# Performance work log

Measured on AMD Instinct MI355X. Metric: run time of the kernel, lower is better.

Reference implementation:

```python
import jax, jax.numpy as jnp
import numpy as np

V, ENC, D, E = 10000, 2048, 512, 512
B, L = 128, 64


def setup_inputs() -> dict:
    key = jax.random.key(0)
    ks = jax.random.split(key, 12)
    s = lambda *sh: 1.0 / np.sqrt(sh[-1])
    return {
        "global_feats": jax.random.normal(ks[0], (B, ENC), jnp.float32),
        "encoded_captions": jax.random.randint(ks[1], (B, L), 0, V, jnp.int64),
        "caption_lengths": jax.random.randint(ks[2], (B,), 1, L, jnp.int64),
        "W_embed": jax.random.normal(ks[3], (V, E), jnp.float32) * 0.02,
        "W_init": jax.random.normal(ks[4], (D, ENC), jnp.float32) * s(ENC),
        "b_init": jnp.zeros((D,), jnp.float32),
        "W_ih": jax.random.normal(ks[5], (3 * D, E), jnp.float32) * s(E),
        "W_hh": jax.random.normal(ks[6], (3 * D, D), jnp.float32) * s(D),
        "b_ih": jnp.zeros((3 * D,), jnp.float32),
        "b_hh": jnp.zeros((3 * D,), jnp.float32),
        "W_fc": jax.random.normal(ks[7], (V, D), jnp.float32) * s(D),
        "b_fc": jnp.zeros((V,), jnp.float32),
    }


def reference(global_feats, encoded_captions, caption_lengths,
              W_embed, W_init, b_init, W_ih, W_hh, b_ih, b_hh, W_fc, b_fc):
    # init_hidden: h0 = tanh(Linear(global_feats))  -> (B, D)
    h0 = jnp.tanh(global_feats @ W_init.T + b_init)

    # teacher forcing over timesteps 0..L-2 (PyTorch GRU gate order: r, z, n)
    emb = W_embed[encoded_captions[:, : L - 1]]          # (B, L-1, E)
    gi = jnp.einsum('ble,ge->blg', emb, W_ih) + b_ih     # (B, L-1, 3D) precomputed input gates
    gi = jnp.swapaxes(gi, 0, 1)                          # (L-1, B, 3D) scan over time

    def step(h, gi_t):
        gh = h @ W_hh.T + b_hh                           # (B, 3D)
        i_r, i_z, i_n = jnp.split(gi_t, 3, axis=-1)
        h_r, h_z, h_n = jnp.split(gh, 3, axis=-1)
        r = jax.nn.sigmoid(i_r + h_r)
        z = jax.nn.sigmoid(i_z + h_z)
        n = jnp.tanh(i_n + r * h_n)
        h_new = (1.0 - z) * n + z * h
        return h_new, h_new

    _, hs = jax.lax.scan(step, h0, gi)                   # hs: (L-1, B, D)
    # dropout is identity in eval/reference mode
    logits = jnp.einsum('lbd,vd->blv', hs, W_fc) + b_fc  # (B, L-1, V)
    return logits, caption_lengths - 1
```

## Files before the change

kernel.cpp:

```cpp
#include <hip/hip_runtime.h>
#include <hip/hip_bf16.h>

#define V_    10000
#define ENC_  2048
#define D_    512
#define B_    128
#define L_    64
#define T_    63
#define M_    (B_ * L_ - B_)
#define G_    (3 * D_)
#define LOGITS_SZ ((long)M_ * V_)
#define SCAN_NB 64

typedef __bf16 bf16x8_t __attribute__((ext_vector_type(8)));
typedef float  f32x4_t  __attribute__((ext_vector_type(4)));
typedef short  s16x8_t  __attribute__((ext_vector_type(8)));
typedef unsigned long long ull_t;

typedef __attribute__((address_space(3))) char*       lds_cptr_t;
typedef const __attribute__((address_space(1))) char* glb_cptr_t;

__device__ __forceinline__ void gload_lds16(const void* g, void* l) {
  __builtin_amdgcn_global_load_lds((glb_cptr_t)g, (lds_cptr_t)l, 16, 0, 0);
}
__device__ __forceinline__ float bf2f(short s) {
  return __uint_as_float(((unsigned)(unsigned short)s) << 16);
}
__device__ __forceinline__ short f2bf(float f) {
  __hip_bfloat16 h = __float2bfloat16(f);
  return *reinterpret_cast<short*>(&h);
}
__device__ __forceinline__ s16x8_t cvt8(const float* p) {
  f32x4_t lo = *reinterpret_cast<const f32x4_t*>(p);
  f32x4_t hi = *reinterpret_cast<const f32x4_t*>(p + 4);
  s16x8_t r;
#pragma unroll
  for (int e = 0; e < 4; e++) { r[e] = f2bf(lo[e]); r[4 + e] = f2bf(hi[e]); }
  return r;
}
__device__ __forceinline__ float sigmoidf_(float x) {
  return 1.0f / (1.0f + __expf(-x));
}
__device__ __forceinline__ bf16x8_t lds_frag(const short* p) {
  return __builtin_bit_cast(bf16x8_t, *reinterpret_cast<const s16x8_t*>(p));
}

__global__ void GG_cvt6(const float* __restrict__ whh, __hip_bfloat16* __restrict__ dwhh,
                        const float* __restrict__ wih, __hip_bfloat16* __restrict__ dwih,
                        const float* __restrict__ wemb, __hip_bfloat16* __restrict__ dwemb,
                        const float* __restrict__ winit, __hip_bfloat16* __restrict__ dwinit,
                        const float* __restrict__ gf, __hip_bfloat16* __restrict__ dgf,
                        const float* __restrict__ wfc, __hip_bfloat16* __restrict__ dwfc) {
  const int i = blockIdx.x * blockDim.x + threadIdx.x;
  const float* s; __hip_bfloat16* d; int off;
  if (i < 98304)        { s = whh;   d = dwhh;   off = i; }
  else if (i < 196608)  { s = wih;   d = dwih;   off = i - 98304; }
  else if (i < 836608)  { s = wemb;  d = dwemb;  off = i - 196608; }
  else if (i < 967680)  { s = winit; d = dwinit; off = i - 836608; }
  else if (i < 1000448) { s = gf;    d = dgf;    off = i - 967680; }
  else {
    if (dwfc == nullptr || i >= 1640448) return;
    s = wfc; d = dwfc; off = i - 1000448;
  }
  s16x8_t v = cvt8(s + (long)off * 8);
  *reinterpret_cast<s16x8_t*>(d + (long)off * 8) = v;
}

__global__ __launch_bounds__(256) void GG_prep(
    const __hip_bfloat16* __restrict__ gfB,
    const __hip_bfloat16* __restrict__ WinitB,
    const float* __restrict__ binit,
    __hip_bfloat16* __restrict__ hfull,
    const __hip_bfloat16* __restrict__ WembB,
    const int* __restrict__ cap,
    const __hip_bfloat16* __restrict__ WihB,
    const float* __restrict__ bih,
    __hip_bfloat16* __restrict__ giC,
    const int* __restrict__ lens,
    float* __restrict__ out) {
  __shared__ short smem[2 * 128 * 64];
  short* sA = smem;
  short* sB = smem + 128 * 64;
  const int lane = threadIdx.x & 63;
  const int wave = threadIdx.x >> 6;
  const int srow = lane >> 3;
  const int scolz = ((lane & 7) ^ (srow & 7)) * 8;
  const int fr = lane & 15;
  const int g4 = lane >> 4;
  const int wm = (wave >> 1) * 64;
  const int wn = (wave & 1) * 64;

  if (blockIdx.x >= 760) {
    if (threadIdx.x < B_) out[LOGITS_SZ + threadIdx.x] = (float)(lens[threadIdx.x] - 1);
    return;
  }

  f32x4_t acc[4][4] = {};

  if (blockIdx.x < 4) {
    const int n0 = blockIdx.x * 128;
    const __hip_bfloat16* aptr[4];
    const __hip_bfloat16* bptr[4];
#pragma unroll
    for (int i = 0; i < 4; i++) {
      const int r = (wave * 4 + i) * 8 + srow;
      aptr[i] = gfB + (long)r * ENC_ + scolz;
      bptr[i] = WinitB + (long)(n0 + r) * ENC_ + scolz;
    }
    for (int kt = 0; kt < 32; kt++) {
      __syncthreads();
#pragma unroll
      for (int i = 0; i < 4; i++) {
        const int chunk = wave * 4 + i;
        gload_lds16(aptr[i] + kt * 64, sA + chunk * 512);
        gload_lds16(bptr[i] + kt * 64, sB + chunk * 512);
      }
      __syncthreads();
#pragma unroll
      for (int kk = 0; kk < 2; kk++) {
        const int gsw = ((kk * 4 + g4) ^ (fr & 7)) * 8;
        bf16x8_t a[4], b[4];
#pragma unroll
        for (int i = 0; i < 4; i++) {
          a[i] = lds_frag(sA + (wm + i * 16 + fr) * 64 + gsw);
          b[i] = lds_frag(sB + (wn + i * 16 + fr) * 64 + gsw);
        }
#pragma unroll
        for (int i = 0; i < 4; i++)
#pragma unroll
          for (int j = 0; j < 4; j++)
            acc[i][j] = __builtin_amdgcn_mfma_f32_16x16x32_bf16(a[i], b[j], acc[i][j], 0, 0, 0);
      }
    }
    const int fq = lane >> 4;
#pragma unroll
    for (int j = 0; j < 4; j++) {
      const int n = n0 + wn + j * 16 + fr;
      const float bv = binit[n];
#pragma unroll
      for (int i = 0; i < 4; i++)
#pragma unroll
        for (int rr = 0; rr < 4; rr++) {
          const int m = wm + i * 16 + fq * 4 + rr;
          hfull[(long)m * 64 * 512 + n] = __float2bfloat16(tanhf(acc[i][j][rr] + bv));
        }
    }
    return;
  }

  const int flat = blockIdx.x - 4;
  const int m0 = (flat / 12) * 128;
  const int n0 = (flat % 12) * 128;
  const __hip_bfloat16* aptr[4];
  const __hip_bfloat16* bptr[4];
#pragma unroll
  for (int i = 0; i < 4; i++) {
    const int r = (wave * 4 + i) * 8 + srow;
    const int bt = m0 + r;
    const int bb = bt / 63;
    const int tt = bt - bb * 63;
    aptr[i] = WembB + (long)cap[bb * L_ + tt] * 512 + scolz;
    bptr[i] = WihB + (long)(n0 + r) * 512 + scolz;
  }
  for (int kt = 0; kt < 8; kt++) {
    __syncthreads();
#pragma unroll
    for (int i = 0; i < 4; i++) {
      const int chunk = wave * 4 + i;
      gload_lds16(aptr[i] + kt * 64, sA + chunk * 512);
      gload_lds16(bptr[i] + kt * 64, sB + chunk * 512);
    }
    __syncthreads();
#pragma unroll
    for (int kk = 0; kk < 2; kk++) {
      const int gsw = ((kk * 4 + g4) ^ (fr & 7)) * 8;
      bf16x8_t a[4], b[4];
#pragma unroll
      for (int i = 0; i < 4; i++) {
        a[i] = lds_frag(sA + (wm + i * 16 + fr) * 64 + gsw);
        b[i] = lds_frag(sB + (wn + i * 16 + fr) * 64 + gsw);
      }
#pragma unroll
      for (int i = 0; i < 4; i++)
#pragma unroll
        for (int j = 0; j < 4; j++)
          acc[i][j] = __builtin_amdgcn_mfma_f32_16x16x32_bf16(a[i], b[j], acc[i][j], 0, 0, 0);
    }
  }
  const int fq = lane >> 4;
#pragma unroll
  for (int j = 0; j < 4; j++) {
    const int n = n0 + wn + j * 16 + fr;
    const float bv = bih[n];
#pragma unroll
    for (int i = 0; i < 4; i++)
#pragma unroll
      for (int rr = 0; rr < 4; rr++) {
        const int m = m0 + wm + i * 16 + fq * 4 + rr;
        giC[(long)m * G_ + n] = __float2bfloat16(acc[i][j][rr] + bv);
      }
  }
}

template <bool BBF16>
__global__ __launch_bounds__(512) void GG_gemm_logits(
    const __hip_bfloat16* __restrict__ hfull,
    const void* __restrict__ Bsrc,
    const float* __restrict__ bias,
    float* __restrict__ C) {
  const int flat = blockIdx.x;
  const int xcd = flat & 7;
  const int s = flat >> 3;
  const int col = xcd * 5 + s % 5;
  const int row = s / 5;
  const int m0 = row * 128;
  const int n0 = col * 256;

  __shared__ short sA[128 * 64];
  __shared__ short sB[256 * 64];
  const int lane = threadIdx.x & 63;
  const int wave = threadIdx.x >> 6;
  const int srow = lane >> 3;
  const int scol  = (lane & 7) * 8;
  const int scolz = ((lane & 7) ^ (srow & 7)) * 8;

  f32x4_t acc[4][4] = {};

  const __hip_bfloat16* aptr[2];
#pragma unroll
  for (int i = 0; i < 2; i++) {
    const int r = (wave + i * 8) * 8 + srow;
    const int m = m0 + r;
    const int bb = m / 63;
    const int tt = m - bb * 63;
    aptr[i] = hfull + ((long)bb * 64 + tt + 1) * 512 + scolz;
  }
  const __hip_bfloat16* bptrB[4];
  const float* bptrF[4];
#pragma unroll
  for (int i = 0; i < 4; i++) {
    int nrow = n0 + (wave + i * 8) * 8 + srow;
    nrow = (nrow < V_) ? nrow : (V_ - 1);
    if constexpr (BBF16) bptrB[i] = (const __hip_bfloat16*)Bsrc + (long)nrow * 512 + scolz;
    else                 bptrF[i] = (const float*)Bsrc + (long)nrow * 512 + scol;
  }

  const int wm = (wave >> 2) * 64;
  const int wn = (wave & 3) * 64;
  const int fr = lane & 15;
  const int g4 = lane >> 4;

  for (int kt = 0; kt < 8; kt++) {
    s16x8_t vb[4];
    if constexpr (!BBF16) {
#pragma unroll
      for (int i = 0; i < 4; i++) vb[i] = cvt8(bptrF[i] + kt * 64);
    }
    __syncthreads();
#pragma unroll
    for (int i = 0; i < 2; i++)
      gload_lds16(aptr[i] + kt * 64, sA + (wave + i * 8) * 512);
#pragma unroll
    for (int i = 0; i < 4; i++) {
      if constexpr (BBF16)
        gload_lds16(bptrB[i] + kt * 64, sB + (wave + i * 8) * 512);
      else
        *reinterpret_cast<s16x8_t*>(
            sB + (wave + i * 8) * 512 + srow * 64 + (((lane & 7) ^ (srow & 7)) * 8)) = vb[i];
    }
    __syncthreads();
#pragma unroll
    for (int kk = 0; kk < 2; kk++) {
      const int gsw = ((kk * 4 + g4) ^ (fr & 7)) * 8;
      bf16x8_t a[4], b[4];
#pragma unroll
      for (int i = 0; i < 4; i++) {
        a[i] = lds_frag(sA + (wm + i * 16 + fr) * 64 + gsw);
        b[i] = lds_frag(sB + (wn + i * 16 + fr) * 64 + gsw);
      }
#pragma unroll
      for (int i = 0; i < 4; i++)
#pragma unroll
        for (int j = 0; j < 4; j++)
          acc[i][j] = __builtin_amdgcn_mfma_f32_16x16x32_bf16(a[i], b[j], acc[i][j], 0, 0, 0);
    }
  }

  const int fq = lane >> 4;
#pragma unroll
  for (int j = 0; j < 4; j++) {
    const int n = n0 + wn + j * 16 + fr;
    if (n >= V_) continue;
    const float bv = bias[n];
#pragma unroll
    for (int i = 0; i < 4; i++)
#pragma unroll
      for (int rr = 0; rr < 4; rr++) {
        const int m = m0 + wm + i * 16 + fq * 4 + rr;
        C[(long)m * V_ + n] = acc[i][j][rr] + bv;
      }
  }
}

__global__ __launch_bounds__(256) void GG_scan_persist(
    __hip_bfloat16* __restrict__ hfull,
    const __hip_bfloat16* __restrict__ gi,
    const __hip_bfloat16* __restrict__ WhhB,
    const float* __restrict__ bhh,
    int* __restrict__ flagbase) {
  __shared__ short sW[48 * 512];
  const int lane = threadIdx.x & 63;
  const int wave = threadIdx.x >> 6;
  const int strip = blockIdx.x & 31;
  const int half  = blockIdx.x >> 5;
  const int d0 = strip * 16;
  const int fr = lane & 15;
  const int g4 = lane >> 4;
  int* myflags = flagbase + half * 32;

  for (int rr = wave; rr < 48; rr += 4) {
    const int grow = (rr >> 4) * 512 + d0 + (rr & 15);
    gload_lds16(WhhB + (long)grow * 512 + (lane ^ (rr & 7)) * 8, sW + rr * 512);
  }

  const int dd = d0 + fr;
  const int bbase = half * 64 + wave * 16 + g4 * 4;
  const float br_ = bhh[dd], bz_ = bhh[512 + dd], bn_ = bhh[1024 + dd];
  const short* gis = (const short*)gi;

  const int arow = half * 64 + wave * 16 + fr;
  const ull_t abase0 =
      (ull_t)hfull + ((ull_t)arow * 64 * 512 + (unsigned)(g4 * 8)) * 2ull;

  ull_t sbase[4];
  const short* gp0[4];
#pragma unroll
  for (int rr = 0; rr < 4; rr++) {
    sbase[rr] = (ull_t)hfull +
                ((ull_t)(bbase + rr) * 64 * 512 + (unsigned)dd) * 2ull;
    gp0[rr] = gis + (long)(bbase + rr) * T_ * G_ + dd;
  }

  unsigned cr[4], cz[4], cn[4];
  float hp[4];
#pragma unroll
  for (int rr = 0; rr < 4; rr++) {
    cr[rr] = (unsigned short)gp0[rr][0];
    cz[rr] = (unsigned short)gp0[rr][512];
    cn[rr] = (unsigned short)gp0[rr][1024];
    hp[rr] = bf2f(*(const short*)&hfull[((long)(bbase + rr) * 64) * 512 + dd]);
  }

  asm volatile("s_waitcnt vmcnt(0)" ::: "memory");
  __syncthreads();

  for (int t = 0; t < T_; t++) {
    if (t > 0) {
      while (true) {
        const int v = __hip_atomic_load(&myflags[lane & 31], __ATOMIC_RELAXED,
                                        __HIP_MEMORY_SCOPE_SYSTEM);
        if (__all(v >= t)) break;
        __builtin_amdgcn_s_sleep(1);
      }
    }

    const ull_t ab = abase0 + (ull_t)t * 1024ull;
    f32x4_t a[16];
#define ALOAD(IDX, OFF)                                                        \
    asm volatile("global_load_dwordx4 %0, %1, off offset:" #OFF " sc0 sc1"     \
                 : "=v"(a[IDX]) : "v"(ab));
    ALOAD(0, 0)    ALOAD(1, 64)   ALOAD(2, 128)  ALOAD(3, 192)
    ALOAD(4, 256)  ALOAD(5, 320)  ALOAD(6, 384)  ALOAD(7, 448)
    ALOAD(8, 512)  ALOAD(9, 576)  ALOAD(10, 640) ALOAD(11, 704)
    ALOAD(12, 768) ALOAD(13, 832) ALOAD(14, 896) ALOAD(15, 960)
#undef ALOAD

    const int tp = (t < T_ - 1) ? (t + 1) : (T_ - 1);
    unsigned nr[4], nz[4], nn[4];
#pragma unroll
    for (int rr = 0; rr < 4; rr++) {
      const short* gp = gp0[rr] + (long)tp * G_;
      asm volatile("global_load_ushort %0, %1, off"             : "=v"(nr[rr]) : "v"(gp));
      asm volatile("global_load_ushort %0, %1, off offset:1024" : "=v"(nz[rr]) : "v"(gp));
      asm volatile("global_load_ushort %0, %1, off offset:2048" : "=v"(nn[rr]) : "v"(gp));
    }

    asm volatile("s_waitcnt vmcnt(12)" ::: "memory");
    __builtin_amdgcn_sched_barrier(0);

    f32x4_t acc[3] = {};
#pragma unroll
    for (int kt = 0; kt < 16; kt++) {
      const bf16x8_t afr = __builtin_bit_cast(bf16x8_t, a[kt]);
      const int gsw = ((kt * 4 + g4) ^ (fr & 7)) * 8;
      bf16x8_t bfr[3];
#pragma unroll
      for (int j = 0; j < 3; j++) bfr[j] = lds_frag(sW + (j * 16 + fr) * 512 + gsw);
#pragma unroll
      for (int j = 0; j < 3; j++)
        acc[j] = __builtin_amdgcn_mfma_f32_16x16x32_bf16(afr, bfr[j], acc[j], 0, 0, 0);
    }

#pragma unroll
    for (int rr = 0; rr < 4; rr++) {
      const float rg = sigmoidf_(bf2f((short)cr[rr]) + acc[0][rr] + br_);
      const float zg = sigmoidf_(bf2f((short)cz[rr]) + acc[1][rr] + bz_);
      const float ng = tanhf(bf2f((short)cn[rr]) + rg * (acc[2][rr] + bn_));
      const short hnb = f2bf((1.f - zg) * ng + zg * hp[rr]);
      hp[rr] = bf2f(hnb);
      const ull_t saddr = sbase[rr] + (ull_t)(t + 1) * 1024ull;
      const unsigned int val = (unsigned short)hnb;
      asm volatile("global_store_short %0, %1, off sc0 sc1"
                   :: "v"(saddr), "v"(val) : "memory");
    }

    asm volatile("s_waitcnt vmcnt(0)" ::: "memory");
    __builtin_amdgcn_sched_barrier(0);
#pragma unroll
    for (int rr = 0; rr < 4; rr++) { cr[rr] = nr[rr]; cz[rr] = nz[rr]; cn[rr] = nn[rr]; }

    if (t < T_ - 1) {
      __syncthreads();
      if (threadIdx.x == 0)
        __hip_atomic_store(&myflags[strip], t + 1, __ATOMIC_RELAXED,
                           __HIP_MEMORY_SCOPE_SYSTEM);
    }
  }
}

extern "C" void kernel_launch(void* const* d_in, const int* in_sizes, int n_in,
                              void* d_out, int out_size, void* d_ws, size_t ws_size,
                              hipStream_t stream) {
  const float* gf      = (const float*)d_in[0];
  const int*   cap     = (const int*)d_in[1];
  const int*   lens    = (const int*)d_in[2];
  const float* W_embed = (const float*)d_in[3];
  const float* W_init  = (const float*)d_in[4];
  const float* b_init  = (const float*)d_in[5];
  const float* W_ih    = (const float*)d_in[6];
  const float* W_hh    = (const float*)d_in[7];
  const float* b_ih    = (const float*)d_in[8];
  const float* b_hh    = (const float*)d_in[9];
  const float* W_fc    = (const float*)d_in[10];
  const float* b_fc    = (const float*)d_in[11];
  float* out = (float*)d_out;

  char* ob = (char*)d_out;
  __hip_bfloat16* gi_ws  = (__hip_bfloat16*)ob;
  __hip_bfloat16* WhhB   = (__hip_bfloat16*)(ob + 25165824);
  __hip_bfloat16* WihB   = (__hip_bfloat16*)(ob + 27262976);
  __hip_bfloat16* WembB  = (__hip_bfloat16*)(ob + 29360128);
  __hip_bfloat16* WinitB = (__hip_bfloat16*)(ob + 40894464);
  __hip_bfloat16* gfB    = (__hip_bfloat16*)(ob + 43253760);

  __hip_bfloat16* hfull = (__hip_bfloat16*)d_ws;
  __hip_bfloat16* WfcB  = (__hip_bfloat16*)((char*)d_ws + 8388608);
  const bool big_ws = ws_size >= (size_t)(8388608 + 10240000 + 256);
  int* flags = (int*)((char*)d_ws + (big_ws ? 18628608 : 8388608));

  hipMemsetAsync(flags, 0, 256, stream);

  GG_cvt6<<<dim3(6408), 256, 0, stream>>>(W_hh, WhhB, W_ih, WihB, W_embed, WembB,
                                          W_init, WinitB, gf, gfB,
                                          W_fc, big_ws ? WfcB : nullptr);

  GG_prep<<<dim3(761), 256, 0, stream>>>(gfB, WinitB, b_init, hfull,
                                         WembB, cap, WihB, b_ih, gi_ws, lens, out);

  GG_scan_persist<<<dim3(SCAN_NB), 256, 0, stream>>>(hfull, gi_ws, WhhB, b_hh, flags);

  if (big_ws)
    GG_gemm_logits<true><<<dim3(2520), 512, 0, stream>>>(hfull, WfcB, b_fc, out);
  else
    GG_gemm_logits<false><<<dim3(2520), 512, 0, stream>>>(hfull, W_fc, b_fc, out);
}
```

Measured before the change: 492.6 us.

## Fuse input-gate GEMM, h0 init and GRU scan into one persistent kernel

Merges the prep kernel (h0 init GEMM and gi projection GEMM) and the persistent scan into a single launch. gi is re-laid out time-major (t, b, gate), and each timestep's gi tiles publish a per-timestep counter, so scan blocks can start once h0 and gi for step 0 are ready and overlap the remaining gi GEMM with the recurrence. This removes one launch boundary and the wait for the whole gi GEMM to finish. In exchange it adds spin-waits and LLC-coherent loads and stores, and it relies on the 64 scan blocks (the lowest block indices) being co-resident with the producer blocks to avoid deadlock.

Measured after the change: 541.4 us. 1.1x slower.

```diff
diff --git a/kernel.cpp b/kernel.cpp
--- a/kernel.cpp
+++ b/kernel.cpp
@@ -10,7 +10,10 @@
 #define M_    (B_ * L_ - B_)
 #define G_    (3 * D_)
 #define LOGITS_SZ ((long)M_ * V_)
-#define SCAN_NB 64
+#define NB_SCAN 64
+#define NB_GI   756
+#define NB_H0   4
+#define NB_ALL  (NB_SCAN + NB_GI + NB_H0 + 1)
 
 typedef __bf16 bf16x8_t __attribute__((ext_vector_type(8)));
 typedef float  f32x4_t  __attribute__((ext_vector_type(4)));
@@ -43,6 +46,15 @@
 }
 __device__ __forceinline__ bf16x8_t lds_frag(const short* p) {
   return __builtin_bit_cast(bf16x8_t, *reinterpret_cast<const s16x8_t*>(p));
+}
+__device__ __forceinline__ void store_short_llc(ull_t addr, unsigned val) {
+  asm volatile("global_store_short %0, %1, off sc0 sc1"
+               :: "v"(addr), "v"(val) : "memory");
+}
+__device__ __forceinline__ unsigned load_ushort_llc(const void* p) {
+  unsigned v;
+  asm volatile("global_load_ushort %0, %1, off sc0 sc1" : "=v"(v) : "v"(p));
+  return v;
 }
 
 __global__ void GG_cvt6(const float* __restrict__ whh, __hip_bfloat16* __restrict__ dwhh,
@@ -66,142 +78,6 @@
   *reinterpret_cast<s16x8_t*>(d + (long)off * 8) = v;
 }
 
-__global__ __launch_bounds__(256) void GG_prep(
-    const __hip_bfloat16* __restrict__ gfB,
-    const __hip_bfloat16* __restrict__ WinitB,
-    const float* __restrict__ binit,
-    __hip_bfloat16* __restrict__ hfull,
-    const __hip_bfloat16* __restrict__ WembB,
-    const int* __restrict__ cap,
-    const __hip_bfloat16* __restrict__ WihB,
-    const float* __restrict__ bih,
-    __hip_bfloat16* __restrict__ giC,
-    const int* __restrict__ lens,
-    float* __restrict__ out) {
-  __shared__ short smem[2 * 128 * 64];
-  short* sA = smem;
-  short* sB = smem + 128 * 64;
-  const int lane = threadIdx.x & 63;
-  const int wave = threadIdx.x >> 6;
-  const int srow = lane >> 3;
-  const int scolz = ((lane & 7) ^ (srow & 7)) * 8;
-  const int fr = lane & 15;
-  const int g4 = lane >> 4;
-  const int wm = (wave >> 1) * 64;
-  const int wn = (wave & 1) * 64;
-
-  if (blockIdx.x >= 760) {
-    if (threadIdx.x < B_) out[LOGITS_SZ + threadIdx.x] = (float)(lens[threadIdx.x] - 1);
-    return;
-  }
-
-  f32x4_t acc[4][4] = {};
-
-  if (blockIdx.x < 4) {
-    const int n0 = blockIdx.x * 128;
-    const __hip_bfloat16* aptr[4];
-    const __hip_bfloat16* bptr[4];
-#pragma unroll
-    for (int i = 0; i < 4; i++) {
-      const int r = (wave * 4 + i) * 8 + srow;
-      aptr[i] = gfB + (long)r * ENC_ + scolz;
-      bptr[i] = WinitB + (long)(n0 + r) * ENC_ + scolz;
-    }
-    for (int kt = 0; kt < 32; kt++) {
-      __syncthreads();
-#pragma unroll
-      for (int i = 0; i < 4; i++) {
-        const int chunk = wave * 4 + i;
-        gload_lds16(aptr[i] + kt * 64, sA + chunk * 512);
-        gload_lds16(bptr[i] + kt * 64, sB + chunk * 512);
-      }
-      __syncthreads();
-#pragma unroll
-      for (int kk = 0; kk < 2; kk++) {
-        const int gsw = ((kk * 4 + g4) ^ (fr & 7)) * 8;
-        bf16x8_t a[4], b[4];
-#pragma unroll
-        for (int i = 0; i < 4; i++) {
-          a[i] = lds_frag(sA + (wm + i * 16 + fr) * 64 + gsw);
-          b[i] = lds_frag(sB + (wn + i * 16 + fr) * 64 + gsw);
-        }
-#pragma unroll
-        for (int i = 0; i < 4; i++)
-#pragma unroll
-          for (int j = 0; j < 4; j++)
-            acc[i][j] = __builtin_amdgcn_mfma_f32_16x16x32_bf16(a[i], b[j], acc[i][j], 0, 0, 0);
-      }
-    }
-    const int fq = lane >> 4;
-#pragma unroll
-    for (int j = 0; j < 4; j++) {
-      const int n = n0 + wn + j * 16 + fr;
-      const float bv = binit[n];
-#pragma unroll
-      for (int i = 0; i < 4; i++)
-#pragma unroll
-        for (int rr = 0; rr < 4; rr++) {
-          const int m = wm + i * 16 + fq * 4 + rr;
-          hfull[(long)m * 64 * 512 + n] = __float2bfloat16(tanhf(acc[i][j][rr] + bv));
-        }
-    }
-    return;
-  }
-
-  const int flat = blockIdx.x - 4;
-  const int m0 = (flat / 12) * 128;
-  const int n0 = (flat % 12) * 128;
-  const __hip_bfloat16* aptr[4];
-  const __hip_bfloat16* bptr[4];
-#pragma unroll
-  for (int i = 0; i < 4; i++) {
-    const int r = (wave * 4 + i) * 8 + srow;
-    const int bt = m0 + r;
-    const int bb = bt / 63;
-    const int tt = bt - bb * 63;
-    aptr[i] = WembB + (long)cap[bb * L_ + tt] * 512 + scolz;
-    bptr[i] = WihB + (long)(n0 + r) * 512 + scolz;
-  }
-  for (int kt = 0; kt < 8; kt++) {
-    __syncthreads();
-#pragma unroll
-    for (int i = 0; i < 4; i++) {
-      const int chunk = wave * 4 + i;
-      gload_lds16(aptr[i] + kt * 64, sA + chunk * 512);
-      gload_lds16(bptr[i] + kt * 64, sB + chunk * 512);
-    }
-    __syncthreads();
-#pragma unroll
-    for (int kk = 0; kk < 2; kk++) {
-      const int gsw = ((kk * 4 + g4) ^ (fr & 7)) * 8;
-      bf16x8_t a[4], b[4];
-#pragma unroll
-      for (int i = 0; i < 4; i++) {
-        a[i] = lds_frag(sA + (wm + i * 16 + fr) * 64 + gsw);
-        b[i] = lds_frag(sB + (wn + i * 16 + fr) * 64 + gsw);
-      }
-#pragma unroll
-      for (int i = 0; i < 4; i++)
-#pragma unroll
-        for (int j = 0; j < 4; j++)
-          acc[i][j] = __builtin_amdgcn_mfma_f32_16x16x32_bf16(a[i], b[j], acc[i][j], 0, 0, 0);
-    }
-  }
-  const int fq = lane >> 4;
-#pragma unroll
-  for (int j = 0; j < 4; j++) {
-    const int n = n0 + wn + j * 16 + fr;
-    const float bv = bih[n];
-#pragma unroll
-    for (int i = 0; i < 4; i++)
-#pragma unroll
-      for (int rr = 0; rr < 4; rr++) {
-        const int m = m0 + wm + i * 16 + fq * 4 + rr;
-        giC[(long)m * G_ + n] = __float2bfloat16(acc[i][j][rr] + bv);
-      }
-  }
-}
-
 template <bool BBF16>
 __global__ __launch_bounds__(512) void GG_gemm_logits(
     const __hip_bfloat16* __restrict__ hfull,
@@ -302,130 +178,287 @@
   }
 }
 
-__global__ __launch_bounds__(256) void GG_scan_persist(
+__global__ __launch_bounds__(256) void GG_mega(
     __hip_bfloat16* __restrict__ hfull,
-    const __hip_bfloat16* __restrict__ gi,
+    __hip_bfloat16* __restrict__ gi,
     const __hip_bfloat16* __restrict__ WhhB,
     const float* __restrict__ bhh,
-    int* __restrict__ flagbase) {
-  __shared__ short sW[48 * 512];
+    int* __restrict__ flags,
+    const __hip_bfloat16* __restrict__ gfB,
+    const __hip_bfloat16* __restrict__ WinitB,
+    const float* __restrict__ binit,
+    const __hip_bfloat16* __restrict__ WembB,
+    const int* __restrict__ cap,
+    const __hip_bfloat16* __restrict__ WihB,
+    const float* __restrict__ bih,
+    const int* __restrict__ lens,
+    float* __restrict__ out) {
+  __shared__ short smem[48 * 512];
   const int lane = threadIdx.x & 63;
   const int wave = threadIdx.x >> 6;
-  const int strip = blockIdx.x & 31;
-  const int half  = blockIdx.x >> 5;
-  const int d0 = strip * 16;
   const int fr = lane & 15;
   const int g4 = lane >> 4;
-  int* myflags = flagbase + half * 32;
-
-  for (int rr = wave; rr < 48; rr += 4) {
-    const int grow = (rr >> 4) * 512 + d0 + (rr & 15);
-    gload_lds16(WhhB + (long)grow * 512 + (lane ^ (rr & 7)) * 8, sW + rr * 512);
-  }
-
-  const int dd = d0 + fr;
-  const int bbase = half * 64 + wave * 16 + g4 * 4;
-  const float br_ = bhh[dd], bz_ = bhh[512 + dd], bn_ = bhh[1024 + dd];
-  const short* gis = (const short*)gi;
-
-  const int arow = half * 64 + wave * 16 + fr;
-  const ull_t abase0 =
-      (ull_t)hfull + ((ull_t)arow * 64 * 512 + (unsigned)(g4 * 8)) * 2ull;
-
-  ull_t sbase[4];
-  const short* gp0[4];
-#pragma unroll
-  for (int rr = 0; rr < 4; rr++) {
-    sbase[rr] = (ull_t)hfull +
-                ((ull_t)(bbase + rr) * 64 * 512 + (unsigned)dd) * 2ull;
-    gp0[rr] = gis + (long)(bbase + rr) * T_ * G_ + dd;
-  }
-
-  unsigned cr[4], cz[4], cn[4];
-  float hp[4];
-#pragma unroll
-  for (int rr = 0; rr < 4; rr++) {
-    cr[rr] = (unsigned short)gp0[rr][0];
-    cz[rr] = (unsigned short)gp0[rr][512];
-    cn[rr] = (unsigned short)gp0[rr][1024];
-    hp[rr] = bf2f(*(const short*)&hfull[((long)(bbase + rr) * 64) * 512 + dd]);
-  }
-
+  int* gicnt = flags + 64;
+  int* h0cnt = flags + 127;
+
+  if (blockIdx.x < NB_SCAN) {
+    short* sW = smem;
+    const int strip = blockIdx.x & 31;
+    const int half  = blockIdx.x >> 5;
+    const int d0 = strip * 16;
+    int* myflags = flags + half * 32;
+
+    for (int rr = wave; rr < 48; rr += 4) {
+      const int grow = (rr >> 4) * 512 + d0 + (rr & 15);
+      gload_lds16(WhhB + (long)grow * 512 + (lane ^ (rr & 7)) * 8, sW + rr * 512);
+    }
+
+    const int dd = d0 + fr;
+    const int bbase = half * 64 + wave * 16 + g4 * 4;
+    const float br_ = bhh[dd], bz_ = bhh[512 + dd], bn_ = bhh[1024 + dd];
+    const short* gis = (const short*)gi;
+
+    const int arow = half * 64 + wave * 16 + fr;
+    const ull_t abase0 =
+        (ull_t)hfull + ((ull_t)arow * 64 * 512 + (unsigned)(g4 * 8)) * 2ull;
+
+    ull_t sbase[4];
+    const short* gp0[4];
+#pragma unroll
+    for (int rr = 0; rr < 4; rr++) {
+      sbase[rr] = (ull_t)hfull +
+                  ((ull_t)(bbase + rr) * 64 * 512 + (unsigned)dd) * 2ull;
+      gp0[rr] = gis + (long)(bbase + rr) * G_ + dd;
+    }
+
+    while (__hip_atomic_load(h0cnt, __ATOMIC_RELAXED, __HIP_MEMORY_SCOPE_SYSTEM) < NB_H0)
+      __builtin_amdgcn_s_sleep(8);
+    float hp[4];
+    unsigned hpu[4];
+#pragma unroll
+    for (int rr = 0; rr < 4; rr++)
+      hpu[rr] = load_ushort_llc((const char*)hfull +
+                                ((long)(bbase + rr) * 64 * 512 + dd) * 2);
+    while (__hip_atomic_load(&gicnt[0], __ATOMIC_RELAXED, __HIP_MEMORY_SCOPE_SYSTEM) < 12)
+      __builtin_amdgcn_s_sleep(8);
+    unsigned cr[4], cz[4], cn[4];
+#pragma unroll
+    for (int rr = 0; rr < 4; rr++) {
+      const short* gp = gp0[rr];
+      cr[rr] = load_ushort_llc(gp);
+      cz[rr] = load_ushort_llc(gp + 512);
+      cn[rr] = load_ushort_llc(gp + 1024);
+    }
+    asm volatile("s_waitcnt vmcnt(0)" ::: "memory");
+#pragma unroll
+    for (int rr = 0; rr < 4; rr++) hp[rr] = bf2f((short)hpu[rr]);
+    __syncthreads();
+
+    for (int t = 0; t < T_; t++) {
+      {
+        const bool needg = (t < T_ - 1);
+        while (true) {
+          int hok = 1;
+          if (t > 0) {
+            const int v = __hip_atomic_load(&myflags[lane & 31], __ATOMIC_RELAXED,
+                                            __HIP_MEMORY_SCOPE_SYSTEM);
+            hok = __all(v >= t) ? 1 : 0;
+          }
+          int gok = 1;
+          if (needg)
+            gok = (__hip_atomic_load(&gicnt[t + 1], __ATOMIC_RELAXED,
+                                     __HIP_MEMORY_SCOPE_SYSTEM) >= 12) ? 1 : 0;
+          if (hok && gok) break;
+          __builtin_amdgcn_s_sleep(1);
+        }
+      }
+
+      const ull_t ab = abase0 + (ull_t)t * 1024ull;
+      f32x4_t a[16];
+#define ALOAD(IDX, OFF)                                                        \
+      asm volatile("global_load_dwordx4 %0, %1, off offset:" #OFF " sc0 sc1"   \
+                   : "=v"(a[IDX]) : "v"(ab));
+      ALOAD(0, 0)    ALOAD(1, 64)   ALOAD(2, 128)  ALOAD(3, 192)
+      ALOAD(4, 256)  ALOAD(5, 320)  ALOAD(6, 384)  ALOAD(7, 448)
+      ALOAD(8, 512)  ALOAD(9, 576)  ALOAD(10, 640) ALOAD(11, 704)
+      ALOAD(12, 768) ALOAD(13, 832) ALOAD(14, 896) ALOAD(15, 960)
+#undef ALOAD
+
+      const int tp = (t < T_ - 1) ? (t + 1) : (T_ - 1);
+      unsigned nr[4], nz[4], nn[4];
+#pragma unroll
+      for (int rr = 0; rr < 4; rr++) {
+        const short* gp = gp0[rr] + (long)tp * (B_ * G_);
+        nr[rr] = load_ushort_llc(gp);
+        nz[rr] = load_ushort_llc(gp + 512);
+        nn[rr] = load_ushort_llc(gp + 1024);
+      }
+
+      asm volatile("s_waitcnt vmcnt(12)" ::: "memory");
+      __builtin_amdgcn_sched_barrier(0);
+
+      f32x4_t acc[3] = {};
+#pragma unroll
+      for (int kt = 0; kt < 16; kt++) {
+        const bf16x8_t afr = __builtin_bit_cast(bf16x8_t, a[kt]);
+        const int gsw = ((kt * 4 + g4) ^ (fr & 7)) * 8;
+        bf16x8_t bfr[3];
+#pragma unroll
+        for (int j = 0; j < 3; j++) bfr[j] = lds_frag(sW + (j * 16 + fr) * 512 + gsw);
+#pragma unroll
+        for (int j = 0; j < 3; j++)
+          acc[j] = __builtin_amdgcn_mfma_f32_16x16x32_bf16(afr, bfr[j], acc[j], 0, 0, 0);
+      }
+
+#pragma unroll
+      for (int rr = 0; rr < 4; rr++) {
+        const float rg = sigmoidf_(bf2f((short)cr[rr]) + acc[0][rr] + br_);
+        const float zg = sigmoidf_(bf2f((short)cz[rr]) + acc[1][rr] + bz_);
+        const float ng = tanhf(bf2f((short)cn[rr]) + rg * (acc[2][rr] + bn_));
+        const short hnb = f2bf((1.f - zg) * ng + zg * hp[rr]);
+        hp[rr] = bf2f(hnb);
+        store_short_llc(sbase[rr] + (ull_t)(t + 1) * 1024ull, (unsigned short)hnb);
+      }
+
+      asm volatile("s_waitcnt vmcnt(0)" ::: "memory");
+      __builtin_amdgcn_sched_barrier(0);
+#pragma unroll
+      for (int rr = 0; rr < 4; rr++) { cr[rr] = nr[rr]; cz[rr] = nz[rr]; cn[rr] = nn[rr]; }
+
+      if (t < T_ - 1) {
+        __syncthreads();
+        if (threadIdx.x == 0)
+          __hip_atomic_store(&myflags[strip], t + 1, __ATOMIC_RELAXED,
+                             __HIP_MEMORY_SCOPE_SYSTEM);
+      }
+    }
+    return;
+  }
+
+  if (blockIdx.x >= NB_SCAN + NB_GI + NB_H0) {
+    if (threadIdx.x < B_) out[LOGITS_SZ + threadIdx.x] = (float)(lens[threadIdx.x] - 1);
+    return;
+  }
+
+  short* sA = smem;
+  short* sB = smem + 128 * 64;
+  const int srow = lane >> 3;
+  const int scolz = ((lane & 7) ^ (srow & 7)) * 8;
+  const int wm = (wave >> 1) * 64;
+  const int wn = (wave & 1) * 64;
+  f32x4_t acc[4][4] = {};
+  const int fq = lane >> 4;
+
+  if (blockIdx.x >= NB_SCAN + NB_GI) {
+    const int n0 = (blockIdx.x - NB_SCAN - NB_GI) * 128;
+    const __hip_bfloat16* aptr[4];
+    const __hip_bfloat16* bptr[4];
+#pragma unroll
+    for (int i = 0; i < 4; i++) {
+      const int r = (wave * 4 + i) * 8 + srow;
+      aptr[i] = gfB + (long)r * ENC_ + scolz;
+      bptr[i] = WinitB + (long)(n0 + r) * ENC_ + scolz;
+    }
+    for (int kt = 0; kt < 32; kt++) {
+      __syncthreads();
+#pragma unroll
+      for (int i = 0; i < 4; i++) {
+        const int chunk = wave * 4 + i;
+        gload_lds16(aptr[i] + kt * 64, sA + chunk * 512);
+        gload_lds16(bptr[i] + kt * 64, sB + chunk * 512);
+      }
+      __syncthreads();
+#pragma unroll
+      for (int kk = 0; kk < 2; kk++) {
+        const int gsw = ((kk * 4 + g4) ^ (fr & 7)) * 8;
+        bf16x8_t a[4], b[4];
+#pragma unroll
+        for (int i = 0; i < 4; i++) {
+          a[i] = lds_frag(sA + (wm + i * 16 + fr) * 64 + gsw);
+          b[i] = lds_frag(sB + (wn + i * 16 + fr) * 64 + gsw);
+        }
+#pragma unroll
+        for (int i = 0; i < 4; i++)
+#pragma unroll
+          for (int j = 0; j < 4; j++)
+            acc[i][j] = __builtin_amdgcn_mfma_f32_16x16x32_bf16(a[i], b[j], acc[i][j], 0, 0, 0);
+      }
+    }
+#pragma unroll
+    for (int j = 0; j < 4; j++) {
+      const int n = n0 + wn + j * 16 + fr;
+      const float bv = binit[n];
+#pragma unroll
+      for (int i = 0; i < 4; i++)
+#pragma unroll
+        for (int rr = 0; rr < 4; rr++) {
+          const int m = wm + i * 16 + fq * 4 + rr;
+          const short hv = f2bf(tanhf(acc[i][j][rr] + bv));
+          store_short_llc((ull_t)hfull + ((ull_t)m * 64 * 512 + n) * 2ull,
+                          (unsigned short)hv);
+        }
+    }
+    asm volatile("s_waitcnt vmcnt(0)" ::: "memory");
+    __syncthreads();
+    if (threadIdx.x == 0)
+      __hip_atomic_fetch_add(h0cnt, 1, __ATOMIC_RELAXED, __HIP_MEMORY_SCOPE_SYSTEM);
+    return;
+  }
+
+  const int flat = blockIdx.x - NB_SCAN;
+  const int tt = flat / 12;
+  const int n0 = (flat % 12) * 128;
+  const __hip_bfloat16* aptr[4];
+  const __hip_bfloat16* bptr[4];
+#pragma unroll
+  for (int i = 0; i < 4; i++) {
+    const int b = (wave * 4 + i) * 8 + srow;
+    aptr[i] = WembB + (long)cap[b * L_ + tt] * 512 + scolz;
+    bptr[i] = WihB + (long)(n0 + (wave * 4 + i) * 8 + srow) * 512 + scolz;
+  }
+  for (int kt = 0; kt < 8; kt++) {
+    __syncthreads();
+#pragma unroll
+    for (int i = 0; i < 4; i++) {
+      const int chunk = wave * 4 + i;
+      gload_lds16(aptr[i] + kt * 64, sA + chunk * 512);
+      gload_lds16(bptr[i] + kt * 64, sB + chunk * 512);
+    }
+    __syncthreads();
+#pragma unroll
+    for (int kk = 0; kk < 2; kk++) {
+      const int gsw = ((kk * 4 + g4) ^ (fr & 7)) * 8;
+      bf16x8_t a[4], b[4];
+#pragma unroll
+      for (int i = 0; i < 4; i++) {
+        a[i] = lds_frag(sA + (wm + i * 16 + fr) * 64 + gsw);
+        b[i] = lds_frag(sB + (wn + i * 16 + fr) * 64 + gsw);
+      }
+#pragma unroll
+      for (int i = 0; i < 4; i++)
+#pragma unroll
+        for (int j = 0; j < 4; j++)
+          acc[i][j] = __builtin_amdgcn_mfma_f32_16x16x32_bf16(a[i], b[j], acc[i][j], 0, 0, 0);
+    }
+  }
+#pragma unroll
+  for (int j = 0; j < 4; j++) {
+    const int n = n0 + wn + j * 16 + fr;
+    const float bv = bih[n];
+#pragma unroll
+    for (int i = 0; i < 4; i++)
+#pragma unroll
+      for (int rr = 0; rr < 4; rr++) {
+        const int b = wm + i * 16 + fq * 4 + rr;
+        const short gv = f2bf(acc[i][j][rr] + bv);
+        store_short_llc((ull_t)gi + (((ull_t)tt * B_ + b) * G_ + n) * 2ull,
+                        (unsigned short)gv);
+      }
+  }
   asm volatile("s_waitcnt vmcnt(0)" ::: "memory");
   __syncthreads();
-
-  for (int t = 0; t < T_; t++) {
-    if (t > 0) {
-      while (true) {
-        const int v = __hip_atomic_load(&myflags[lane & 31], __ATOMIC_RELAXED,
-                                        __HIP_MEMORY_SCOPE_SYSTEM);
-        if (__all(v >= t)) break;
-        __builtin_amdgcn_s_sleep(1);
-      }
-    }
-
-    const ull_t ab = abase0 + (ull_t)t * 1024ull;
-    f32x4_t a[16];
-#define ALOAD(IDX, OFF)                                                        \
-    asm volatile("global_load_dwordx4 %0, %1, off offset:" #OFF " sc0 sc1"     \
-                 : "=v"(a[IDX]) : "v"(ab));
-    ALOAD(0, 0)    ALOAD(1, 64)   ALOAD(2, 128)  ALOAD(3, 192)
-    ALOAD(4, 256)  ALOAD(5, 320)  ALOAD(6, 384)  ALOAD(7, 448)
-    ALOAD(8, 512)  ALOAD(9, 576)  ALOAD(10, 640) ALOAD(11, 704)
-    ALOAD(12, 768) ALOAD(13, 832) ALOAD(14, 896) ALOAD(15, 960)
-#undef ALOAD
-
-    const int tp = (t < T_ - 1) ? (t + 1) : (T_ - 1);
-    unsigned nr[4], nz[4], nn[4];
-#pragma unroll
-    for (int rr = 0; rr < 4; rr++) {
-      const short* gp = gp0[rr] + (long)tp * G_;
-      asm volatile("global_load_ushort %0, %1, off"             : "=v"(nr[rr]) : "v"(gp));
-      asm volatile("global_load_ushort %0, %1, off offset:1024" : "=v"(nz[rr]) : "v"(gp));
-      asm volatile("global_load_ushort %0, %1, off offset:2048" : "=v"(nn[rr]) : "v"(gp));
-    }
-
-    asm volatile("s_waitcnt vmcnt(12)" ::: "memory");
-    __builtin_amdgcn_sched_barrier(0);
-
-    f32x4_t acc[3] = {};
-#pragma unroll
-    for (int kt = 0; kt < 16; kt++) {
-      const bf16x8_t afr = __builtin_bit_cast(bf16x8_t, a[kt]);
-      const int gsw = ((kt * 4 + g4) ^ (fr & 7)) * 8;
-      bf16x8_t bfr[3];
-#pragma unroll
-      for (int j = 0; j < 3; j++) bfr[j] = lds_frag(sW + (j * 16 + fr) * 512 + gsw);
-#pragma unroll
-      for (int j = 0; j < 3; j++)
-        acc[j] = __builtin_amdgcn_mfma_f32_16x16x32_bf16(afr, bfr[j], acc[j], 0, 0, 0);
-    }
-
-#pragma unroll
-    for (int rr = 0; rr < 4; rr++) {
-      const float rg = sigmoidf_(bf2f((short)cr[rr]) + acc[0][rr] + br_);
-      const float zg = sigmoidf_(bf2f((short)cz[rr]) + acc[1][rr] + bz_);
-      const float ng = tanhf(bf2f((short)cn[rr]) + rg * (acc[2][rr] + bn_));
-      const short hnb = f2bf((1.f - zg) * ng + zg * hp[rr]);
-      hp[rr] = bf2f(hnb);
-      const ull_t saddr = sbase[rr] + (ull_t)(t + 1) * 1024ull;
-      const unsigned int val = (unsigned short)hnb;
-      asm volatile("global_store_short %0, %1, off sc0 sc1"
-                   :: "v"(saddr), "v"(val) : "memory");
-    }
-
-    asm volatile("s_waitcnt vmcnt(0)" ::: "memory");
-    __builtin_amdgcn_sched_barrier(0);
-#pragma unroll
-    for (int rr = 0; rr < 4; rr++) { cr[rr] = nr[rr]; cz[rr] = nz[rr]; cn[rr] = nn[rr]; }
-
-    if (t < T_ - 1) {
-      __syncthreads();
-      if (threadIdx.x == 0)
-        __hip_atomic_store(&myflags[strip], t + 1, __ATOMIC_RELAXED,
-                           __HIP_MEMORY_SCOPE_SYSTEM);
-    }
-  }
+  if (threadIdx.x == 0)
+    __hip_atomic_fetch_add(&gicnt[tt], 1, __ATOMIC_RELAXED, __HIP_MEMORY_SCOPE_SYSTEM);
 }
 
 extern "C" void kernel_launch(void* const* d_in, const int* in_sizes, int n_in,
@@ -455,19 +488,18 @@
 
   __hip_bfloat16* hfull = (__hip_bfloat16*)d_ws;
   __hip_bfloat16* WfcB  = (__hip_bfloat16*)((char*)d_ws + 8388608);
-  const bool big_ws = ws_size >= (size_t)(8388608 + 10240000 + 256);
+  const bool big_ws = ws_size >= (size_t)(8388608 + 10240000 + 512);
   int* flags = (int*)((char*)d_ws + (big_ws ? 18628608 : 8388608));
 
-  hipMemsetAsync(flags, 0, 256, stream);
+  hipMemsetAsync(flags, 0, 512, stream);
 
   GG_cvt6<<<dim3(6408), 256, 0, stream>>>(W_hh, WhhB, W_ih, WihB, W_embed, WembB,
                                           W_init, WinitB, gf, gfB,
                                           W_fc, big_ws ? WfcB : nullptr);
 
-  GG_prep<<<dim3(761), 256, 0, stream>>>(gfB, WinitB, b_init, hfull,
-                                         WembB, cap, WihB, b_ih, gi_ws, lens, out);
-
-  GG_scan_persist<<<dim3(SCAN_NB), 256, 0, stream>>>(hfull, gi_ws, WhhB, b_hh, flags);
+  GG_mega<<<dim3(NB_ALL), 256, 0, stream>>>(hfull, gi_ws, WhhB, b_hh, flags,
+                                            gfB, WinitB, b_init,
+                                            WembB, cap, WihB, b_ih, lens, out);
 
   if (big_ws)
     GG_gemm_logits<true><<<dim3(2520), 512, 0, stream>>>(hfull, WfcB, b_fc, out);
```
